# Performance work log

Hardware: AMD Instinct MI355X
Metric: run time of the kernel (lower is better)

The kernel has to match this reference:

```python
import jax, jax.numpy as jnp
import numpy as np

# Fixed production-scale dims (equal-size graphs -> no ragged padding needed)
B, NPG, C, H, L, FFN, NC = 16, 512, 128, 8, 4, 512, 4
D = C // H          # head dim = 16
T = NPG + 1         # +1 virtual graph token
EPG = 8192          # edges per graph (avg degree 16)
E = B * EPG


def _ln(x, g, b, eps=1e-5):
    m = x.mean(-1, keepdims=True)
    v = ((x - m) ** 2).mean(-1, keepdims=True)
    return (x - m) * jax.lax.rsqrt(v + eps) * g + b


def setup_inputs() -> dict:
    key = jax.random.key(0)
    ks = jax.random.split(key, 24)
    N = B * NPG
    node_feats = jax.random.normal(ks[0], (N, 3), jnp.float32)
    # intra-graph edges: local endpoints + per-graph node offset (matches batch_ptr math)
    local = jax.random.randint(ks[1], (2, B, EPG), 0, NPG)
    offs = (jnp.arange(B) * NPG)[None, :, None]
    edge_index = (local + offs).reshape(2, E)
    edge_attr = jax.random.randint(ks[2], (E,), 0, 10)

    def nrm(k, shape, scale=0.02):
        return jax.random.normal(k, shape, jnp.float32) * scale

    params = {
        "W_node": nrm(ks[3], (3, C), 0.3), "b_node": jnp.zeros((C,), jnp.float32),
        "graph_token": nrm(ks[4], (C,), 1.0),
        "edge_bias_table": nrm(ks[5], (11, H), 0.1).at[0].set(0.0),  # padding_idx=0
        "in_deg_emb": nrm(ks[6], (512, C)).at[0].set(0.0),           # padding_idx=0
        "out_deg_emb": nrm(ks[7], (512, C)).at[0].set(0.0),
        "vnode_bias": nrm(ks[8], (H,), 1.0),
        "Wq": nrm(ks[9], (L, C, C)), "bq": jnp.zeros((L, C), jnp.float32),
        "Wk": nrm(ks[10], (L, C, C)), "bk": jnp.zeros((L, C), jnp.float32),
        "Wv": nrm(ks[11], (L, C, C)), "bv": jnp.zeros((L, C), jnp.float32),
        "Wo": nrm(ks[12], (L, C, C)), "bo": jnp.zeros((L, C), jnp.float32),
        "ln1_g": jnp.ones((L, C), jnp.float32), "ln1_b": jnp.zeros((L, C), jnp.float32),
        "ln2_g": jnp.ones((L, C), jnp.float32), "ln2_b": jnp.zeros((L, C), jnp.float32),
        "W1": nrm(ks[13], (L, C, FFN)), "b1": jnp.zeros((L, FFN), jnp.float32),
        "W2": nrm(ks[14], (L, FFN, C)), "b2": jnp.zeros((L, C), jnp.float32),
        "normf_g": jnp.ones((C,), jnp.float32), "normf_b": jnp.zeros((C,), jnp.float32),
        "Wc1": nrm(ks[15], (C, C // 2)), "bc1": jnp.zeros((C // 2,), jnp.float32),
        "Wc2": nrm(ks[16], (C // 2, NC)), "bc2": jnp.zeros((NC,), jnp.float32),
    }
    return {"node_feats": node_feats, "edge_index": edge_index,
            "edge_attr": edge_attr, "num_graphs": B, **params}


def reference(node_feats, W_node, b_node, graph_token, edge_bias_table,
              in_deg_emb, out_deg_emb, vnode_bias,
              Wq, bq, Wk, bk, Wv, bv, Wo, bo,
              ln1_g, ln1_b, ln2_g, ln2_b, W1, b1, W2, b2,
              normf_g, normf_b, Wc1, bc1, Wc2, bc2,
              edge_index, edge_attr, num_graphs):
    N = node_feats.shape[0]
    npg = N // num_graphs
    t = npg + 1
    src, dst = edge_index[0], edge_index[1]
    # degree encoders (scatter_add of ones == segment_sum)
    in_deg = jnp.clip(jax.ops.segment_sum(jnp.ones_like(dst), dst, num_segments=N), 0, 511)
    out_deg = jnp.clip(jax.ops.segment_sum(jnp.ones_like(src), src, num_segments=N), 0, 511)
    x_enc = node_feats @ W_node + b_node + in_deg_emb[in_deg] + out_deg_emb[out_deg]
    # equal-size graphs with sorted batch ids -> padding loop is a reshape, mask all-False
    x = jnp.concatenate(
        [jnp.broadcast_to(graph_token, (num_graphs, 1, C)),
         x_enc.reshape(num_graphs, npg, C)], axis=1)  # [B, T, C]
    # attention bias: vnode row/col + scattered edge-attr embeddings
    bias = jnp.zeros((num_graphs, H, t, t), jnp.float32)
    bias = bias.at[:, :, 0, :].set(vnode_bias[None, :, None])
    bias = bias.at[:, :, :, 0].set(vnode_bias[None, :, None])
    eb = edge_bias_table[jnp.clip(edge_attr, 0, 9) + 1]  # [E, H]
    g = src // npg
    sl = src - g * npg + 1
    dl = dst - g * npg + 1
    bias = bias.at[g, :, sl, dl].add(eb)  # duplicate edges accumulate (scatter_add)
    scale = 1.0 / np.sqrt(D).astype(np.float32)
    for l in range(L):  # key_padding_mask is all-False here -> masked_fill is a no-op
        h = _ln(x, ln1_g[l], ln1_b[l])
        q = (h @ Wq[l] + bq[l]).reshape(num_graphs, t, H, D)
        k = (h @ Wk[l] + bk[l]).reshape(num_graphs, t, H, D)
        v = (h @ Wv[l] + bv[l]).reshape(num_graphs, t, H, D)
        scores = jnp.einsum('bthd,bshd->bhts', q, k) * scale + bias
        attn = jax.nn.softmax(scores, axis=-1)
        o = jnp.einsum('bhts,bshd->bthd', attn, v).reshape(num_graphs, t, C)
        x = x + o @ Wo[l] + bo[l]
        h2 = _ln(x, ln2_g[l], ln2_b[l])
        x = x + jax.nn.gelu(h2 @ W1[l] + b1[l], approximate=False) @ W2[l] + b2[l]
    x = _ln(x, normf_g, normf_b)
    gr = x[:, 0, :]  # virtual-node readout
    return jax.nn.gelu(gr @ Wc1 + bc1, approximate=False) @ Wc2 + bc2
```

## Files before the change

### kernel.cpp

```cpp
#include <hip/hip_runtime.h>
#include <hip/hip_bf16.h>

#define BB 16
#define NPG 512
#define CC 128
#define HH 8
#define LL 4
#define FFN 512
#define NCLS 4
#define DD 16
#define TT 513
#define EE 131072
#define NNODES 8192
#define ROWS (BB * TT)
#define ECAP 64
#define SP 544
#define SSTR 548

static constexpr size_t XROWS = (size_t)BB * TT;
static constexpr size_t XSZ   = XROWS * CC;
static constexpr size_t VTSZ  = (size_t)BB * HH * DD * SP;

typedef unsigned short ushort_t;
typedef __attribute__((ext_vector_type(8))) short short8;
typedef __attribute__((ext_vector_type(4))) float floatx4;

__device__ __forceinline__ float gelu_exact(float v) {
    return 0.5f * v * (1.0f + erff(v * 0.70710678118654752440f));
}
__device__ __forceinline__ ushort_t f2bf(float f) {
    union { float f; unsigned u; } c; c.f = f;
    unsigned u = c.u;
    return (ushort_t)((u + 0x7FFFu + ((u >> 16) & 1u)) >> 16);
}
__device__ __forceinline__ int swz(int row, int col, int stride) {
    int kb = col >> 3;
    return row * stride + (((kb ^ (row & 7)) << 3) | (col & 7));
}

__device__ __forceinline__ void qkv_stage8(const ushort_t* hs,
                                           const ushort_t* Wtq, const float* bq_,
                                           const ushort_t* Wtk, const float* bk_,
                                           const ushort_t* Wtv, const float* bv_,
                                           ushort_t* qh, ushort_t* kh, ushort_t* vt,
                                           int b, int t0, int wave, int lq, int quad) {
    const short* hsS = (const short*)hs;
    int c = wave * 16 + lq;
    const short* Ws[3] = {(const short*)Wtq, (const short*)Wtk, (const short*)Wtv};
    const float* bs[3] = {bq_, bk_, bv_};
    size_t rB = (size_t)c * CC;

    #pragma unroll
    for (int m = 0; m < 3; ++m) {
        const short* W = Ws[m];
        floatx4 a0 = {0.f,0.f,0.f,0.f};
        #pragma unroll
        for (int k0 = 0; k0 < CC; k0 += 32) {
            short8 af = *(const short8*)(hsS + swz(lq, k0 + quad * 8, 128));
            short8 b0 = *(const short8*)(W + rB + k0 + quad * 8);
            a0 = __builtin_amdgcn_mfma_f32_16x16x32_bf16(af, b0, a0, 0, 0, 0);
        }
        float bv0 = bs[m][c];
        #pragma unroll
        for (int rg = 0; rg < 4; ++rg) {
            int t = t0 + quad * 4 + rg;
            if (t >= TT) continue;
            float v0 = a0[rg] + bv0;
            size_t hr = ((size_t)(b * HH + wave) * TT + t) * DD + lq;
            if (m == 0) {
                qh[hr] = f2bf(v0 * 0.25f);
            } else if (m == 1) {
                kh[hr] = f2bf(v0);
            } else {
                vt[((size_t)(b * HH + wave) * DD + lq) * SP + t] = f2bf(v0);
            }
        }
    }
}

__global__ __launch_bounds__(256) void deg_csr_tr_kernel(const int* __restrict__ ei,
                                                         const int* __restrict__ ea,
                                                         int* __restrict__ deg_in,
                                                         int* __restrict__ deg_out,
                                                         int* __restrict__ cnt,
                                                         int* __restrict__ ebuf,
                                                         const float* __restrict__ Wq,
                                                         const float* __restrict__ Wk,
                                                         const float* __restrict__ Wv,
                                                         const float* __restrict__ Wo,
                                                         const float* __restrict__ W1,
                                                         const float* __restrict__ W2,
                                                         ushort_t* __restrict__ wtqkvo,
                                                         ushort_t* __restrict__ wt1,
                                                         ushort_t* __restrict__ wt2) {
    int bid = blockIdx.x;
    int tid = threadIdx.x;
    if (bid < 512) {
        int e = bid * 256 + tid;
        int src = ei[e], dst = ei[EE + e];
        atomicAdd(&deg_out[src], 1);
        atomicAdd(&deg_in[dst], 1);
        int g = src >> 9;
        int sl = src - (g << 9) + 1;
        int dl = dst - (g << 9) + 1;
        int a = ea[e];
        a = (a < 0) ? 0 : (a > 9 ? 9 : a);
        a += 1;
        int row = g * TT + sl;
        int pos = atomicAdd(&cnt[row], 1);
        if (pos < ECAP) ebuf[(size_t)row * ECAP + pos] = dl | (a << 16);
        return;
    }
    int z = bid - 512;
    const float* src; ushort_t* dst; int K, N, tile;
    if (z < 64) {
        int zz = z >> 2; tile = z & 3;
        int k = zz >> 2, l = zz & 3;
        const float* s4[4] = {Wq, Wk, Wv, Wo};
        src = s4[k] + (size_t)l * CC * CC;
        dst = wtqkvo + (size_t)(k * 4 + l) * 16384;
        K = CC; N = CC;
    } else if (z < 128) {
        int l = (z - 64) >> 4; tile = (z - 64) & 15;
        src = W1 + (size_t)l * CC * FFN;
        dst = wt1 + (size_t)l * 65536;
        K = CC; N = FFN;
    } else {
        int l = (z - 128) >> 4; tile = (z - 128) & 15;
        src = W2 + (size_t)l * FFN * CC;
        dst = wt2 + (size_t)l * 65536;
        K = FFN; N = CC;
    }
    int tilesN = N >> 6;
    int k0 = (tile / tilesN) << 6;
    int n0 = (tile - (tile / tilesN) * tilesN) << 6;
    __shared__ float t[64][65];
    int c = tid & 63, rb = tid >> 6;
    #pragma unroll
    for (int kk = 0; kk < 64; kk += 4)
        t[kk + rb][c] = src[(size_t)(k0 + kk + rb) * N + n0 + c];
    __syncthreads();
    #pragma unroll
    for (int nn = 0; nn < 64; nn += 4)
        dst[(size_t)(n0 + nn + rb) * K + k0 + c] = f2bf(t[c][nn + rb]);
}

__global__ __launch_bounds__(512) void pre_kernel(const float* __restrict__ nf,
                                                  const float* __restrict__ Wn,
                                                  const float* __restrict__ bn,
                                                  const float* __restrict__ gt,
                                                  const float* __restrict__ ide,
                                                  const float* __restrict__ ode,
                                                  const int* __restrict__ deg_in,
                                                  const int* __restrict__ deg_out,
                                                  const float* __restrict__ ln1g_,
                                                  const float* __restrict__ ln1b_,
                                                  const ushort_t* __restrict__ wtqkvo,
                                                  const float* __restrict__ bq_,
                                                  const float* __restrict__ bk_,
                                                  const float* __restrict__ bv_,
                                                  float* __restrict__ x_,
                                                  ushort_t* __restrict__ qh,
                                                  ushort_t* __restrict__ kh,
                                                  ushort_t* __restrict__ vt) {
    int bid = blockIdx.x;
    int tid = threadIdx.x;
    int b = bid / 33, qt = bid - b * 33;
    int t0 = qt * 16;
    int wave = tid >> 6, lane = tid & 63, lq = lane & 15, quad = lane >> 4;

    __shared__ ushort_t hs[16 * 128];
    __shared__ float sred[8][16][2];

    int c = wave * 16 + lq;
    float w0[4];
    #pragma unroll
    for (int rg = 0; rg < 4; ++rg) {
        int t = t0 + quad * 4 + rg;
        int tc = min(t, TT - 1);
        float v0;
        if (tc == 0) {
            v0 = gt[c];
        } else {
            int i = b * NPG + tc - 1;
            float f0 = nf[i*3+0], f1 = nf[i*3+1], f2 = nf[i*3+2];
            v0 = bn[c] + f0*Wn[0*CC + c] + f1*Wn[1*CC + c] + f2*Wn[2*CC + c];
            int di = min(deg_in[i], 511);
            int dq = min(deg_out[i], 511);
            v0 += ide[(size_t)di * CC + c] + ode[(size_t)dq * CC + c];
        }
        if (t < TT) x_[((size_t)b * TT + t) * CC + c] = v0;
        w0[rg] = v0;
    }
    #pragma unroll
    for (int rg = 0; rg < 4; ++rg) {
        float s1 = w0[rg];
        float s2 = w0[rg] * w0[rg];
        #pragma unroll
        for (int m = 1; m < 16; m <<= 1) {
            s1 += __shfl_xor(s1, m, 64);
            s2 += __shfl_xor(s2, m, 64);
        }
        if (lq == 0) { sred[wave][quad*4+rg][0] = s1; sred[wave][quad*4+rg][1] = s2; }
    }
    __syncthreads();
    float g0 = ln1g_[c], lb0 = ln1b_[c];
    #pragma unroll
    for (int rg = 0; rg < 4; ++rg) {
        int row = quad * 4 + rg;
        float S1 = 0.f, S2 = 0.f;
        #pragma unroll
        for (int w = 0; w < 8; ++w) { S1 += sred[w][row][0]; S2 += sred[w][row][1]; }
        float mn = S1 * (1.0f/CC);
        float var = S2 * (1.0f/CC) - mn * mn;
        float rs = rsqrtf(var + 1e-5f);
        hs[swz(row, c, 128)] = f2bf((w0[rg] - mn) * rs * g0 + lb0);
    }
    __syncthreads();
    qkv_stage8(hs, wtqkvo, bq_,
               wtqkvo + (size_t)4 * 16384, bk_,
               wtqkvo + (size_t)8 * 16384, bv_,
               qh, kh, vt, b, t0, wave, lq, quad);
}

__global__ __launch_bounds__(256, 4) void attn_kernel(const ushort_t* __restrict__ qhr,
                                                      const ushort_t* __restrict__ khr,
                                                      const ushort_t* __restrict__ vtr,
                                                      const int* __restrict__ cnt,
                                                      const int* __restrict__ ebuf,
                                                      const float* __restrict__ ebt,
                                                      const float* __restrict__ vnode,
                                                      ushort_t* __restrict__ obf) {
    int qt = blockIdx.x;
    int bh = blockIdx.y;
    int b = bh >> 3, h = bh & (HH - 1);
    int tid = threadIdx.x;
    int wave = tid >> 6, lane = tid & 63, lq = lane & 15, quad = lane >> 4;

    __shared__ __align__(16) float strip[16 * SSTR];
    __shared__ __align__(16) int elist[16 * 64];
    __shared__ float ebtl[12];
    __shared__ int cn_s[16];

    for (int i = tid; i < 16 * SSTR / 4; i += 256)
        ((float4*)strip)[i] = make_float4(0.f, 0.f, 0.f, 0.f);
    if (tid < 11) ebtl[tid] = ebt[tid * 8 + h];
    {
        int r = tid >> 4, j4 = (tid & 15) * 4;
        int qrow = qt * 16 + r;
        bool rv = (qrow >= 1) && (qrow < TT);
        size_t crow = (size_t)b * TT + (rv ? qrow : 0);
        *(int4*)&elist[r * 64 + j4] = *(const int4*)(ebuf + crow * ECAP + j4);
        if ((tid & 15) == 0) cn_s[r] = rv ? min(cnt[crow], ECAP) : 0;
    }
    __syncthreads();
    if (tid < 16) {
        int qrow = qt * 16 + tid;
        if (qrow >= 1 && qrow < TT) strip[tid * SSTR] = vnode[h];
    }
    {
        int r = tid >> 4;
        int cn = cn_s[r];
        for (int j = tid & 15; j < cn; j += 16) {
            int e = elist[r * 64 + j];
            atomicAdd(&strip[r * SSTR + (e & 0xFFFF)], ebtl[e >> 16]);
        }
    }
    __syncthreads();

    int qg = qt * 16 + lq;
    int qr = min(qg, TT - 1);
    short8 z8 = {0,0,0,0,0,0,0,0};
    const short* qhS = (const short*)qhr;
    const short* khS = (const short*)khr;
    short8 qf = z8;
    if (quad < 2)
        qf = *(const short8*)(qhS + ((size_t)bh * TT + qr) * DD + quad * 8);
    const short* vtS = (const short*)(vtr + (size_t)bh * DD * SP);

    floatx4 oacc = {0.f, 0.f, 0.f, 0.f};
    float lsum = 0.f;

    short8 af0c = z8, af1c = z8, vfc;
    {
        int sp = wave;
        int t0r = min(sp * 2 * 16 + lq, TT - 1);
        int t1r = min((sp * 2 + 1) * 16 + lq, TT - 1);
        if (quad < 2) {
            af0c = *(const short8*)(khS + ((size_t)bh * TT + t0r) * DD + quad * 8);
            af1c = *(const short8*)(khS + ((size_t)bh * TT + t1r) * DD + quad * 8);
        }
        vfc = *(const short8*)(vtS + (size_t)lq * SP + sp * 32 + quad * 8);
    }

    for (int sp = wave; sp < 17; sp += 4) {
        int spn = sp + 4;
        short8 af0n = z8, af1n = z8, vfn = z8;
        if (spn < 17) {
            int t0r = min(spn * 2 * 16 + lq, TT - 1);
            int t1r = min((spn * 2 + 1) * 16 + lq, TT - 1);
            if (quad < 2) {
                af0n = *(const short8*)(khS + ((size_t)bh * TT + t0r) * DD + quad * 8);
                af1n = *(const short8*)(khS + ((size_t)bh * TT + t1r) * DD + quad * 8);
            }
            vfn = *(const short8*)(vtS + (size_t)lq * SP + spn * 32 + quad * 8);
        }

        int roff = lq * SSTR + sp * 32 + quad * 4;
        float4 bia = *(const float4*)&strip[roff];
        float4 bib = *(const float4*)&strip[roff + 16];

        unsigned pw[2][2];
        #pragma unroll
        for (int t = 0; t < 2; ++t) {
            int st = sp * 2 + t;
            floatx4 cc4 = __builtin_amdgcn_mfma_f32_16x16x32_bf16(
                t ? af1c : af0c, qf, (floatx4){0.f, 0.f, 0.f, 0.f}, 0, 0, 0);
            float4 bi = t ? bib : bia;
            float biv[4] = {bi.x, bi.y, bi.z, bi.w};
            float pr[4];
            #pragma unroll
            for (int rg = 0; rg < 4; ++rg) {
                int s = st * 16 + quad * 4 + rg;
                float p = 0.f;
                if (s < TT) p = __expf(cc4[rg] + biv[rg]);
                lsum += p;
                pr[rg] = p;
            }
            pw[t][0] = (unsigned)f2bf(pr[0]) | ((unsigned)f2bf(pr[1]) << 16);
            pw[t][1] = (unsigned)f2bf(pr[2]) | ((unsigned)f2bf(pr[3]) << 16);
        }
        int srcA = lq + (((2 * quad) & 3) << 4);
        int srcB = lq + (((2 * quad + 1) & 3) << 4);
        int a00 = __shfl((int)pw[0][0], srcA, 64);
        int a01 = __shfl((int)pw[0][1], srcA, 64);
        int a10 = __shfl((int)pw[1][0], srcA, 64);
        int a11 = __shfl((int)pw[1][1], srcA, 64);
        int b00 = __shfl((int)pw[0][0], srcB, 64);
        int b01 = __shfl((int)pw[0][1], srcB, 64);
        int b10 = __shfl((int)pw[1][0], srcB, 64);
        int b11 = __shfl((int)pw[1][1], srcB, 64);
        union { int u[4]; short8 s8; } pu;
        bool lo = quad < 2;
        pu.u[0] = lo ? a00 : a10;
        pu.u[1] = lo ? a01 : a11;
        pu.u[2] = lo ? b00 : b10;
        pu.u[3] = lo ? b01 : b11;
        oacc = __builtin_amdgcn_mfma_f32_16x16x32_bf16(vfc, pu.s8, oacc, 0, 0, 0);

        af0c = af0n; af1c = af1n; vfc = vfn;
    }

    lsum += __shfl_xor(lsum, 16, 64);
    lsum += __shfl_xor(lsum, 32, 64);
    __syncthreads();
    float* redw = strip;
    float* lsumS = strip + 1088;
    #pragma unroll
    for (int rg = 0; rg < 4; ++rg)
        redw[wave * 272 + (quad * 4 + rg) * 17 + lq] = oacc[rg];
    if (quad == 0) lsumS[wave * 16 + lq] = lsum;
    __syncthreads();
    {
        int q = tid >> 4, d = tid & 15;
        float o = 0.f, L = 0.f;
        #pragma unroll
        for (int w = 0; w < 4; ++w) {
            o += redw[w * 272 + d * 17 + q];
            L += lsumS[w * 16 + q];
        }
        int qq = qt * 16 + q;
        if (qq < TT)
            obf[((size_t)(b * TT + qq)) * CC + h * DD + d] = f2bf(o / L);
    }
}

__global__ __launch_bounds__(512, 4) void mega_kernel(const ushort_t* __restrict__ obf,
                                                      const ushort_t* __restrict__ WtO,
                                                      const float* __restrict__ bo_,
                                                      const float* __restrict__ ln2g_,
                                                      const float* __restrict__ ln2b_,
                                                      const ushort_t* __restrict__ Wt1_,
                                                      const float* __restrict__ b1_,
                                                      const ushort_t* __restrict__ Wt2_,
                                                      const float* __restrict__ b2_,
                                                      const float* __restrict__ ln1g_,
                                                      const float* __restrict__ ln1b_,
                                                      const ushort_t* __restrict__ Wtq,
                                                      const float* __restrict__ bq_,
                                                      const ushort_t* __restrict__ Wtk,
                                                      const float* __restrict__ bk_,
                                                      const ushort_t* __restrict__ Wtv,
                                                      const float* __restrict__ bv_,
                                                      const float* __restrict__ nfg,
                                                      const float* __restrict__ nfb,
                                                      const float* __restrict__ Wc1,
                                                      const float* __restrict__ bc1,
                                                      const float* __restrict__ Wc2,
                                                      const float* __restrict__ bc2,
                                                      float* __restrict__ x_,
                                                      ushort_t* __restrict__ qhw,
                                                      ushort_t* __restrict__ khw,
                                                      ushort_t* __restrict__ vtw,
                                                      float* __restrict__ out,
                                                      int doQKV) {
    int qt = blockIdx.x, b = blockIdx.y;
    int tid = threadIdx.x;
    int wave = tid >> 6, lane = tid & 63, lq = lane & 15, quad = lane >> 4;

    __shared__ __align__(16) ushort_t hs[16 * 128];
    __shared__ __align__(16) ushort_t ms[16 * 512];
    __shared__ float sred[8][16][2];

    int t0 = qt * 16;
    int c = wave * 16 + lq;
    float vv0[4];

    float xr[4];
    #pragma unroll
    for (int rg = 0; rg < 4; ++rg) {
        int t = t0 + quad * 4 + rg;
        xr[rg] = x_[((size_t)b * TT + min(t, TT - 1)) * CC + c];
    }
    const short* W1S = (const short*)Wt1_;
    short8 w2p[8];
    #pragma unroll
    for (int nt = 0; nt < 2; ++nt)
        #pragma unroll
        for (int kk = 0; kk < 4; ++kk)
            w2p[nt*4+kk] = *(const short8*)(W1S + (size_t)(wave * 64 + nt * 16 + lq) * CC
                                            + kk * 32 + quad * 8);

    {
        const short* obS = (const short*)obf;
        size_t arow = (size_t)b * TT + min(t0 + lq, TT - 1);
        const short* W = (const short*)WtO;
        size_t rB = (size_t)c * CC;
        floatx4 a0 = {0.f,0.f,0.f,0.f};
        #pragma unroll
        for (int k0 = 0; k0 < CC; k0 += 32) {
            short8 af = *(const short8*)(obS + arow * CC + k0 + quad * 8);
            short8 b0 = *(const short8*)(W + rB + k0 + quad * 8);
            a0 = __builtin_amdgcn_mfma_f32_16x16x32_bf16(af, b0, a0, 0, 0, 0);
        }
        float bv0 = bo_[c];
        #pragma unroll
        for (int rg = 0; rg < 4; ++rg)
            vv0[rg] = a0[rg] + bv0 + xr[rg];
        #pragma unroll
        for (int rg = 0; rg < 4; ++rg) {
            float s1 = vv0[rg];
            float s2 = vv0[rg] * vv0[rg];
            #pragma unroll
            for (int m = 1; m < 16; m <<= 1) {
                s1 += __shfl_xor(s1, m, 64);
                s2 += __shfl_xor(s2, m, 64);
            }
            if (lq == 0) { sred[wave][quad*4+rg][0] = s1; sred[wave][quad*4+rg][1] = s2; }
        }
        __syncthreads();
        float g0 = ln2g_[c], lb0 = ln2b_[c];
        #pragma unroll
        for (int rg = 0; rg < 4; ++rg) {
            int row = quad * 4 + rg;
            float S1 = 0.f, S2 = 0.f;
            #pragma unroll
            for (int w = 0; w < 8; ++w) { S1 += sred[w][row][0]; S2 += sred[w][row][1]; }
            float mn = S1 * (1.0f/CC);
            float var = S2 * (1.0f/CC) - mn * mn;
            float rs = rsqrtf(var + 1e-5f);
            hs[swz(row, c, 128)] = f2bf((vv0[rg] - mn) * rs * g0 + lb0);
        }
    }
    __syncthreads();

    {
        const short* hsS = (const short*)hs;
        #pragma unroll
        for (int nt = 0; nt < 4; ++nt) {
            int n = wave * 64 + nt * 16;
            size_t rB = (size_t)(n + lq) * CC;
            floatx4 a0 = {0.f,0.f,0.f,0.f};
            #pragma unroll
            for (int kk = 0; kk < 4; ++kk) {
                int k0 = kk * 32;
                short8 af = *(const short8*)(hsS + swz(lq, k0 + quad * 8, 128));
                short8 b0 = (nt < 2) ? w2p[nt*4+kk]
                                     : *(const short8*)(W1S + rB + k0 + quad * 8);
                a0 = __builtin_amdgcn_mfma_f32_16x16x32_bf16(af, b0, a0, 0, 0, 0);
            }
            float bb0 = b1_[n + lq];
            #pragma unroll
            for (int rg = 0; rg < 4; ++rg)
                ms[swz(quad * 4 + rg, n + lq, 512)] = f2bf(gelu_exact(a0[rg] + bb0));
        }
    }
    __syncthreads();

    float w0[4];
    {
        const short* msS = (const short*)ms;
        const short* W = (const short*)Wt2_;
        size_t rB = (size_t)c * FFN;
        floatx4 a0 = {0.f,0.f,0.f,0.f};
        #pragma unroll 8
        for (int k0 = 0; k0 < FFN; k0 += 32) {
            short8 af = *(const short8*)(msS + swz(lq, k0 + quad * 8, 512));
            short8 b0 = *(const short8*)(W + rB + k0 + quad * 8);
            a0 = __builtin_amdgcn_mfma_f32_16x16x32_bf16(af, b0, a0, 0, 0, 0);
        }
        float bv0 = b2_[c];
        #pragma unroll
        for (int rg = 0; rg < 4; ++rg) {
            int t = t0 + quad * 4 + rg;
            w0[rg] = a0[rg] + bv0 + vv0[rg];
            if (t < TT) x_[((size_t)b * TT + t) * CC + c] = w0[rg];
        }
    }

    if (doQKV) {
        #pragma unroll
        for (int rg = 0; rg < 4; ++rg) {
            float s1 = w0[rg];
            float s2 = w0[rg] * w0[rg];
            #pragma unroll
            for (int m = 1; m < 16; m <<= 1) {
                s1 += __shfl_xor(s1, m, 64);
                s2 += __shfl_xor(s2, m, 64);
            }
            if (lq == 0) { sred[wave][quad*4+rg][0] = s1; sred[wave][quad*4+rg][1] = s2; }
        }
        __syncthreads();
        float g0 = ln1g_[c], lb0 = ln1b_[c];
        #pragma unroll
        for (int rg = 0; rg < 4; ++rg) {
            int row = quad * 4 + rg;
            float S1 = 0.f, S2 = 0.f;
            #pragma unroll
            for (int w = 0; w < 8; ++w) { S1 += sred[w][row][0]; S2 += sred[w][row][1]; }
            float mn = S1 * (1.0f/CC);
            float var = S2 * (1.0f/CC) - mn * mn;
            float rs = rsqrtf(var + 1e-5f);
            hs[swz(row, c, 128)] = f2bf((w0[rg] - mn) * rs * g0 + lb0);
        }
        __syncthreads();
        qkv_stage8(hs, Wtq, bq_, Wtk, bk_, Wtv, bv_, qhw, khw, vtw, b, t0, wave, lq, quad);
        return;
    }

    if (qt != 0) return;

    __syncthreads();
    float* hrow = (float*)ms;
    float* xfs  = hrow + CC;
    float* c1s  = xfs + CC;
    float* red  = c1s + 64;
    if (quad == 0) hrow[c] = w0[0];
    __syncthreads();

    {
        int ct = tid;
        float v = 0.f, s1 = 0.f, s2 = 0.f;
        if (ct < CC) { v = hrow[ct]; s1 = v; s2 = v * v; }
        #pragma unroll
        for (int m = 32; m >= 1; m >>= 1) {
            s1 += __shfl_xor(s1, m, 64);
            s2 += __shfl_xor(s2, m, 64);
        }
        int w = ct >> 6;
        if (ct < CC && (ct & 63) == 0) { red[w*2] = s1; red[w*2+1] = s2; }
        __syncthreads();
        if (ct < CC) {
            float S1 = red[0] + red[2], S2 = red[1] + red[3];
            float mn = S1 * (1.0f/CC);
            float var = S2 * (1.0f/CC) - mn * mn;
            float rs = rsqrtf(var + 1e-5f);
            xfs[ct] = (v - mn) * rs * nfg[ct] + nfb[ct];
        }
        __syncthreads();
        if (ct < 64) {
            float acc = bc1[ct];
            #pragma unroll 4
            for (int k = 0; k < CC; ++k) acc = fmaf(xfs[k], Wc1[(size_t)k * 64 + ct], acc);
            c1s[ct] = gelu_exact(acc);
        }
        __syncthreads();
        if (ct < NCLS) {
            float acc = bc2[ct];
            #pragma unroll 4
            for (int j = 0; j < 64; ++j) acc = fmaf(c1s[j], Wc2[(size_t)j * NCLS + ct], acc);
            out[(size_t)b * NCLS + ct] = acc;
        }
    }
}

extern "C" void kernel_launch(void* const* d_in, const int* in_sizes, int n_in,
                              void* d_out, int out_size, void* d_ws, size_t ws_size,
                              hipStream_t stream) {
    const float* node_feats = (const float*)d_in[0];
    const int*   edge_index = (const int*)d_in[1];
    const int*   edge_attr  = (const int*)d_in[2];
    const float* W_node  = (const float*)d_in[4];
    const float* b_node  = (const float*)d_in[5];
    const float* g_token = (const float*)d_in[6];
    const float* ebt     = (const float*)d_in[7];
    const float* ide     = (const float*)d_in[8];
    const float* ode     = (const float*)d_in[9];
    const float* vnode   = (const float*)d_in[10];
    const float* Wq = (const float*)d_in[11];
    const float* bq = (const float*)d_in[12];
    const float* Wk = (const float*)d_in[13];
    const float* bk = (const float*)d_in[14];
    const float* Wv = (const float*)d_in[15];
    const float* bv = (const float*)d_in[16];
    const float* Wo = (const float*)d_in[17];
    const float* bo = (const float*)d_in[18];
    const float* ln1g = (const float*)d_in[19];
    const float* ln1b = (const float*)d_in[20];
    const float* ln2g = (const float*)d_in[21];
    const float* ln2b = (const float*)d_in[22];
    const float* W1 = (const float*)d_in[23];
    const float* b1 = (const float*)d_in[24];
    const float* W2 = (const float*)d_in[25];
    const float* b2 = (const float*)d_in[26];
    const float* nfg = (const float*)d_in[27];
    const float* nfb = (const float*)d_in[28];
    const float* Wc1 = (const float*)d_in[29];
    const float* bc1 = (const float*)d_in[30];
    const float* Wc2 = (const float*)d_in[31];
    const float* bc2 = (const float*)d_in[32];
    float* out = (float*)d_out;

    char* base = (char*)d_ws;
    float* x      = (float*)base;     base += XSZ * 4;
    ushort_t* qh0 = (ushort_t*)base;  base += XSZ * 2;
    ushort_t* kh0 = (ushort_t*)base;  base += XSZ * 2;
    ushort_t* vt0 = (ushort_t*)base;  base += VTSZ * 2;
    ushort_t* qh1 = (ushort_t*)base;  base += XSZ * 2;
    ushort_t* kh1 = (ushort_t*)base;  base += XSZ * 2;
    ushort_t* vt1 = (ushort_t*)base;  base += VTSZ * 2;
    ushort_t* obf = (ushort_t*)base;  base += XSZ * 2;
    ushort_t* wtqkvo = (ushort_t*)base; base += (size_t)16 * 16384 * 2;
    ushort_t* wt1 = (ushort_t*)base;  base += (size_t)4 * 65536 * 2;
    ushort_t* wt2 = (ushort_t*)base;  base += (size_t)4 * 65536 * 2;
    int* deg_in  = (int*)base;        base += NNODES * 4;
    int* deg_out = (int*)base;        base += NNODES * 4;
    int* cnt     = (int*)base;        base += (size_t)ROWS * 4;
    int* ebuf    = (int*)base;        base += (size_t)ROWS * ECAP * 4;

    ushort_t* qhs[2] = {qh0, qh1};
    ushort_t* khs[2] = {kh0, kh1};
    ushort_t* vts[2] = {vt0, vt1};

    hipMemsetAsync(deg_in, 0, (size_t)(2 * NNODES + ROWS) * 4, stream);
    deg_csr_tr_kernel<<<512 + 192, 256, 0, stream>>>(
        edge_index, edge_attr, deg_in, deg_out, cnt, ebuf,
        Wq, Wk, Wv, Wo, W1, W2, wtqkvo, wt1, wt2);

    pre_kernel<<<528, 512, 0, stream>>>(
        node_feats, W_node, b_node, g_token, ide, ode, deg_in, deg_out,
        ln1g, ln1b, wtqkvo, bq, bk, bv, x, qh0, kh0, vt0);

    for (int l = 0; l < LL; ++l) {
        int rd = l & 1, wr = rd ^ 1;
        int ln = (l + 1) % LL;

        attn_kernel<<<dim3(33, BB * HH), 256, 0, stream>>>(
            qhs[rd], khs[rd], vts[rd], cnt, ebuf, ebt, vnode, obf);

        mega_kernel<<<dim3(33, BB), 512, 0, stream>>>(
            obf,
            wtqkvo + (size_t)(12 + l)*16384, bo + l*CC,
            ln2g + l*CC, ln2b + l*CC,
            wt1 + (size_t)l*65536, b1 + l*FFN,
            wt2 + (size_t)l*65536, b2 + l*CC,
            ln1g + ln*CC, ln1b + ln*CC,
            wtqkvo + (size_t)(0 + ln)*16384, bq + ln*CC,
            wtqkvo + (size_t)(4 + ln)*16384, bk + ln*CC,
            wtqkvo + (size_t)(8 + ln)*16384, bv + ln*CC,
            nfg, nfb, Wc1, bc1, Wc2, bc2,
            x, qhs[wr], khs[wr], vts[wr], out,
            (l < LL-1) ? 1 : 0);
    }
}
```

Measured before the change: 446.9 us.

## Halve mega_kernel row tile to 8 rows and double its grid

```diff
diff --git a/kernel.cpp b/kernel.cpp
--- a/kernel.cpp
+++ b/kernel.cpp
@@ -43,7 +43,8 @@
                                            const ushort_t* Wtk, const float* bk_,
                                            const ushort_t* Wtv, const float* bv_,
                                            ushort_t* qh, ushort_t* kh, ushort_t* vt,
-                                           int b, int t0, int wave, int lq, int quad) {
+                                           int b, int t0, int wave, int lq, int quad,
+                                           int rowlim) {
     const short* hsS = (const short*)hs;
     int c = wave * 16 + lq;
     const short* Ws[3] = {(const short*)Wtq, (const short*)Wtk, (const short*)Wtv};
@@ -63,8 +64,9 @@
         float bv0 = bs[m][c];
         #pragma unroll
         for (int rg = 0; rg < 4; ++rg) {
-            int t = t0 + quad * 4 + rg;
-            if (t >= TT) continue;
+            int r8 = quad * 4 + rg;
+            int t = t0 + r8;
+            if (r8 >= rowlim || t >= TT) continue;
             float v0 = a0[rg] + bv0;
             size_t hr = ((size_t)(b * HH + wave) * TT + t) * DD + lq;
             if (m == 0) {
@@ -220,7 +222,7 @@
     qkv_stage8(hs, wtqkvo, bq_,
                wtqkvo + (size_t)4 * 16384, bk_,
                wtqkvo + (size_t)8 * 16384, bv_,
-               qh, kh, vt, b, t0, wave, lq, quad);
+               qh, kh, vt, b, t0, wave, lq, quad, 16);
 }
 
 __global__ __launch_bounds__(256, 4) void attn_kernel(const ushort_t* __restrict__ qhr,
@@ -375,7 +377,7 @@
     }
 }
 
-__global__ __launch_bounds__(512, 4) void mega_kernel(const ushort_t* __restrict__ obf,
+__global__ __launch_bounds__(512, 8) void mega_kernel(const ushort_t* __restrict__ obf,
                                                       const ushort_t* __restrict__ WtO,
                                                       const float* __restrict__ bo_,
                                                       const float* __restrict__ ln2g_,
@@ -412,7 +414,7 @@
     __shared__ __align__(16) ushort_t ms[16 * 512];
     __shared__ float sred[8][16][2];
 
-    int t0 = qt * 16;
+    int t0 = qt * 8;
     int c = wave * 16 + lq;
     float vv0[4];
 
@@ -422,14 +424,6 @@
         int t = t0 + quad * 4 + rg;
         xr[rg] = x_[((size_t)b * TT + min(t, TT - 1)) * CC + c];
     }
-    const short* W1S = (const short*)Wt1_;
-    short8 w2p[8];
-    #pragma unroll
-    for (int nt = 0; nt < 2; ++nt)
-        #pragma unroll
-        for (int kk = 0; kk < 4; ++kk)
-            w2p[nt*4+kk] = *(const short8*)(W1S + (size_t)(wave * 64 + nt * 16 + lq) * CC
-                                            + kk * 32 + quad * 8);
 
     {
         const short* obS = (const short*)obf;
@@ -476,17 +470,16 @@
 
     {
         const short* hsS = (const short*)hs;
+        const short* W = (const short*)Wt1_;
         #pragma unroll
         for (int nt = 0; nt < 4; ++nt) {
             int n = wave * 64 + nt * 16;
             size_t rB = (size_t)(n + lq) * CC;
             floatx4 a0 = {0.f,0.f,0.f,0.f};
             #pragma unroll
-            for (int kk = 0; kk < 4; ++kk) {
-                int k0 = kk * 32;
+            for (int k0 = 0; k0 < CC; k0 += 32) {
                 short8 af = *(const short8*)(hsS + swz(lq, k0 + quad * 8, 128));
-                short8 b0 = (nt < 2) ? w2p[nt*4+kk]
-                                     : *(const short8*)(W1S + rB + k0 + quad * 8);
+                short8 b0 = *(const short8*)(W + rB + k0 + quad * 8);
                 a0 = __builtin_amdgcn_mfma_f32_16x16x32_bf16(af, b0, a0, 0, 0, 0);
             }
             float bb0 = b1_[n + lq];
@@ -512,9 +505,10 @@
         float bv0 = b2_[c];
         #pragma unroll
         for (int rg = 0; rg < 4; ++rg) {
-            int t = t0 + quad * 4 + rg;
+            int r8 = quad * 4 + rg;
+            int t = t0 + r8;
             w0[rg] = a0[rg] + bv0 + vv0[rg];
-            if (t < TT) x_[((size_t)b * TT + t) * CC + c] = w0[rg];
+            if (r8 < 8 && t < TT) x_[((size_t)b * TT + t) * CC + c] = w0[rg];
         }
     }
 
@@ -544,7 +538,7 @@
             hs[swz(row, c, 128)] = f2bf((w0[rg] - mn) * rs * g0 + lb0);
         }
         __syncthreads();
-        qkv_stage8(hs, Wtq, bq_, Wtk, bk_, Wtv, bv_, qhw, khw, vtw, b, t0, wave, lq, quad);
+        qkv_stage8(hs, Wtq, bq_, Wtk, bk_, Wtv, bv_, qhw, khw, vtw, b, t0, wave, lq, quad, 8);
         return;
     }
 
@@ -668,7 +662,7 @@
         attn_kernel<<<dim3(33, BB * HH), 256, 0, stream>>>(
             qhs[rd], khs[rd], vts[rd], cnt, ebuf, ebt, vnode, obf);
 
-        mega_kernel<<<dim3(33, BB), 512, 0, stream>>>(
+        mega_kernel<<<dim3(65, BB), 512, 0, stream>>>(
             obf,
             wtqkvo + (size_t)(12 + l)*16384, bo + l*CC,
             ln2g + l*CC, ln2b + l*CC,
```

After: 563.3 us. 1.26x slower.
